# Kernel optimization log

Measured on AMD Instinct MI355X. Metric: run time of the kernel, lower is better.

The kernel has to match this reference:

```python
import jax, jax.numpy as jnp
import numpy as np

MARGIN = 1.0
N_NODES = 8192
EMBED_DIM = 128
N_COMM = 100


def setup_inputs() -> dict:
    key = jax.random.key(0)
    k1, k2 = jax.random.split(key)
    embeddings = jax.random.normal(k1, (N_NODES, EMBED_DIM), dtype=jnp.float32)
    communities = jax.random.randint(k2, (N_NODES,), 0, N_COMM, dtype=jnp.int64)
    return {"embeddings": embeddings, "communities": communities}


def _cdist(x):
    # Euclidean pairwise distances, sqrt made grad-safe at 0.
    sq = jnp.sum(x * x, axis=1)
    d2 = sq[:, None] + sq[None, :] - 2.0 * (x @ x.T)
    d2 = jnp.maximum(d2, 0.0)
    return jnp.where(d2 > 0, jnp.sqrt(jnp.where(d2 > 0, d2, 1.0)), 0.0)


def reference(embeddings, communities):
    n = embeddings.shape[0]
    dist = _cdist(embeddings)                              # (n, n)
    same = communities[:, None] == communities[None, :]    # (n, n)
    pos_mask = same & ~jnp.eye(n, dtype=bool)              # positives: same comm, j != i
    neg_mask = ~same                                       # negatives: any other community
    inf = jnp.array(jnp.inf, dist.dtype)
    # hardest (closest) negative per anchor row
    min_neg = jnp.min(jnp.where(neg_mask, dist, inf), axis=1)   # (n,)
    has_neg = jnp.any(neg_mask, axis=1)                         # (n,)
    # triplet margin over every (anchor, positive) pair
    tl = jnp.maximum(dist - min_neg[:, None] + MARGIN, 0.0)     # (n, n)
    valid = pos_mask & has_neg[:, None]
    total = jnp.sum(jnp.where(valid, tl, 0.0))
    count = jnp.sum(valid)
    # reduction='mean' over valid triplets; 0.0 if no valid triplets / single community
    return jnp.where(count > 0, total / count.astype(total.dtype), jnp.zeros((), total.dtype))
```

## Files before the change

### kernel.cpp

```cpp
#include <hip/hip_runtime.h>

#define N_NODES 8192
#define DIM     128
#define N_COMM  100
#define MARGIN  1.0f

#define KQ       32
#define LDS_STR  40
#define LDS_STRP 72
#define RP_STR   68

typedef __attribute__((ext_vector_type(8)))  short bf16x8;
typedef __attribute__((ext_vector_type(16))) float f32x16;

__device__ inline unsigned short f32_to_bf16_rne(float f) {
    unsigned u = __float_as_uint(f);
    unsigned r = u + 0x7fffu + ((u >> 16) & 1u);
    return (unsigned short)(r >> 16);
}
__device__ inline float bf16_to_f32(unsigned short h) {
    return __uint_as_float(((unsigned)h) << 16);
}

__global__ __launch_bounds__(256)
void prep_kernel(const float* __restrict__ x,
                 const int* __restrict__ comm,
                 unsigned short* __restrict__ xhi,
                 unsigned short* __restrict__ xlo,
                 float* __restrict__ sq,
                 unsigned int* __restrict__ min_d2,
                 int* __restrict__ offs,
                 int* __restrict__ members) {
    __shared__ int scnt[N_COMM];
    __shared__ int scur[N_COMM];
    const int tid = threadIdx.x;

    if (blockIdx.x < 2048) {
        int row  = blockIdx.x * 4 + (tid >> 6);
        int lane = tid & 63;
        const float* p = x + (size_t)row * DIM;
        float v0 = p[lane], v1 = p[lane + 64];
        unsigned short h0 = f32_to_bf16_rne(v0), h1 = f32_to_bf16_rne(v1);
        unsigned short l0 = f32_to_bf16_rne(v0 - bf16_to_f32(h0));
        unsigned short l1 = f32_to_bf16_rne(v1 - bf16_to_f32(h1));
        size_t base = (size_t)row * DIM;
        xhi[base + lane] = h0;  xhi[base + 64 + lane] = h1;
        xlo[base + lane] = l0;  xlo[base + 64 + lane] = l1;
        float s = v0 * v0 + v1 * v1;
        #pragma unroll
        for (int off = 32; off > 0; off >>= 1) s += __shfl_down(s, off);
        if (lane == 0) {
            sq[row] = s;
            min_d2[row] = 0x7f800000u;
        }
        return;
    }

    if (tid < N_COMM) scnt[tid] = 0;
    __syncthreads();
    for (int i = tid; i < N_NODES; i += 256) atomicAdd(&scnt[comm[i]], 1);
    __syncthreads();
    if (tid == 0) {
        int acc = 0;
        for (int c = 0; c < N_COMM; ++c) { scur[c] = acc; offs[c] = acc; acc += scnt[c]; }
        offs[N_COMM] = acc;
    }
    __syncthreads();
    for (int i = tid; i < N_NODES; i += 256) {
        int p = atomicAdd(&scur[comm[i]], 1);
        members[p] = i;
    }
}

__global__ __launch_bounds__(256, 3)
void minneg_mfma_kernel(const unsigned short* __restrict__ xhi,
                        const unsigned short* __restrict__ xlo,
                        const int* __restrict__ comm,
                        const float* __restrict__ sq,
                        unsigned int* __restrict__ min_d2) {
    __shared__ __align__(16) unsigned short lds[4][128][LDS_STR];
    __shared__ unsigned int colmin[128];

    const int b = blockIdx.x;
    int bx = (int)((sqrtf(8.f * (float)b + 1.f) - 1.f) * 0.5f);
    while ((bx + 1) * (bx + 2) / 2 <= b) ++bx;
    while (bx * (bx + 1) / 2 > b) --bx;
    const int by = b - bx * (bx + 1) / 2;

    const int tid  = threadIdx.x;
    const int lane = tid & 63;
    const int w    = tid >> 6;
    const int wr   = w >> 1, wc = w & 1;
    const int lr   = lane & 31;
    const int lh   = lane >> 5;
    const int i0   = bx * 128;
    const int j0   = by * 128;

    if (tid < 128) colmin[tid] = 0x7f800000u;

    f32x16 acc[2][2];
    #pragma unroll
    for (int g = 0; g < 2; ++g)
        #pragma unroll
        for (int h = 0; h < 2; ++h)
            #pragma unroll
            for (int e = 0; e < 16; ++e) acc[g][h][e] = 0.f;

    #pragma unroll
    for (int kq = 0; kq < 4; ++kq) {
        __syncthreads();
        #pragma unroll
        for (int it = 0; it < 8; ++it) {
            int g    = tid + it * 256;
            int tile = g >> 9;
            int row  = (g >> 2) & 127;
            int seg  = g & 3;
            const unsigned short* src = (tile & 1) ? xlo : xhi;
            int rbase = (tile & 2) ? j0 : i0;
            uint4 v = *(const uint4*)&src[(size_t)(rbase + row) * DIM + kq * KQ + seg * 8];
            *(uint4*)&lds[tile][row][seg * 8] = v;
        }
        __syncthreads();

        #pragma unroll
        for (int ks = 0; ks < 2; ++ks) {
            const int kb = ks * 16 + lh * 8;
            bf16x8 ahi[2], alo[2], bhi[2], blo[2];
            #pragma unroll
            for (int g = 0; g < 2; ++g) {
                ahi[g] = *(const bf16x8*)&lds[0][wr * 64 + g * 32 + lr][kb];
                alo[g] = *(const bf16x8*)&lds[1][wr * 64 + g * 32 + lr][kb];
            }
            #pragma unroll
            for (int h = 0; h < 2; ++h) {
                bhi[h] = *(const bf16x8*)&lds[2][wc * 64 + h * 32 + lr][kb];
                blo[h] = *(const bf16x8*)&lds[3][wc * 64 + h * 32 + lr][kb];
            }
            #pragma unroll
            for (int g = 0; g < 2; ++g)
                #pragma unroll
                for (int h = 0; h < 2; ++h) {
                    acc[g][h] = __builtin_amdgcn_mfma_f32_32x32x16_bf16(
                        ahi[g], bhi[h], acc[g][h], 0, 0, 0);
                    acc[g][h] = __builtin_amdgcn_mfma_f32_32x32x16_bf16(
                        ahi[g], blo[h], acc[g][h], 0, 0, 0);
                    acc[g][h] = __builtin_amdgcn_mfma_f32_32x32x16_bf16(
                        alo[g], bhi[h], acc[g][h], 0, 0, 0);
                }
        }
    }

    int   civ[2][4][4];
    float sqv[2][4][4];
    #pragma unroll
    for (int g = 0; g < 2; ++g)
        #pragma unroll
        for (int q = 0; q < 4; ++q) {
            int rb = i0 + wr * 64 + g * 32 + 4 * lh + 8 * q;
            *(int4*)&civ[g][q][0]   = *(const int4*)&comm[rb];
            *(float4*)&sqv[g][q][0] = *(const float4*)&sq[rb];
        }

    const float FINF = __uint_as_float(0x7f800000u);
    float rmin[2][16];
    #pragma unroll
    for (int g = 0; g < 2; ++g)
        #pragma unroll
        for (int e = 0; e < 16; ++e) rmin[g][e] = FINF;

    #pragma unroll
    for (int h = 0; h < 2; ++h) {
        int colt = wc * 64 + h * 32 + lr;
        int j  = j0 + colt;
        int cj = comm[j];
        float sqj = sq[j];
        float cmin = FINF;
        #pragma unroll
        for (int g = 0; g < 2; ++g)
            #pragma unroll
            for (int q = 0; q < 4; ++q)
                #pragma unroll
                for (int t = 0; t < 4; ++t) {
                    float d2 = fmaxf(sqv[g][q][t] + sqj - 2.f * acc[g][h][q * 4 + t], 0.f);
                    if (civ[g][q][t] != cj) {
                        cmin = fminf(cmin, d2);
                        rmin[g][q * 4 + t] = fminf(rmin[g][q * 4 + t], d2);
                    }
                }
        cmin = fminf(cmin, __shfl_xor(cmin, 32));
        if (lh == 0) atomicMin(&colmin[colt], __float_as_uint(cmin));
    }

    __syncthreads();
    float (*rowpart)[RP_STR] = (float (*)[RP_STR])lds;
    #pragma unroll
    for (int g = 0; g < 2; ++g)
        #pragma unroll
        for (int q = 0; q < 4; ++q)
            #pragma unroll
            for (int t = 0; t < 4; ++t) {
                int rowl = wr * 64 + g * 32 + 4 * lh + 8 * q + t;
                rowpart[rowl][wc * 32 + lr] = rmin[g][q * 4 + t];
            }
    __syncthreads();
    if (tid < 128) {
        float m = FINF;
        #pragma unroll
        for (int k = 0; k < 16; ++k) {
            float4 v = *(const float4*)&rowpart[tid][k * 4];
            m = fminf(m, fminf(fminf(v.x, v.y), fminf(v.z, v.w)));
        }
        atomicMin(&min_d2[i0 + tid], __float_as_uint(m));
        atomicMin(&min_d2[j0 + tid], colmin[tid]);
    }
}

__global__ __launch_bounds__(256, 2)
void pos_mfma_kernel(const unsigned short* __restrict__ xhi,
                     const unsigned short* __restrict__ xlo,
                     const float* __restrict__ sq,
                     const unsigned int* __restrict__ min_d2,
                     const int* __restrict__ offs,
                     const int* __restrict__ members,
                     double* __restrict__ psum,
                     unsigned int* __restrict__ pcnt) {
    __shared__ __align__(16) unsigned short lds[4][128][LDS_STRP];
    __shared__ float sqA[128], sqB[128], mnA[128];
    __shared__ double sred[4];
    __shared__ unsigned int cred[4];

    const int tid  = threadIdx.x;
    const int lane = tid & 63;
    const int w    = tid >> 6;
    const int wr   = w >> 1, wc = w & 1;
    const int lr   = lane & 31;
    const int lh   = lane >> 5;

    const int c    = blockIdx.x;
    const int beg  = offs[c], end = offs[c + 1];
    const int size = end - beg;
    const int nt   = (size + 127) >> 7;

    float tsum = 0.f;
    unsigned int tcnt = 0u;

    for (int tr = 0; tr < nt; ++tr)
    for (int tc = 0; tc < nt; ++tc) {
        bool av[2], bv[2];
        #pragma unroll
        for (int g = 0; g < 2; ++g) av[g] = (tr * 128 + wr * 64 + g * 32) < size;
        #pragma unroll
        for (int h = 0; h < 2; ++h) bv[h] = (tc * 128 + wc * 64 + h * 32) < size;

        __syncthreads();
        if (tid < 128) {
            int ii = beg + tr * 128 + tid;
            if (ii < end) {
                int ia = members[ii];
                sqA[tid] = sq[ia];
                unsigned int mb = min_d2[ia];
                mnA[tid] = (mb == 0x7f800000u) ? -1.f
                         : sqrtf(fmaxf(__uint_as_float(mb), 0.f));
            } else { sqA[tid] = 0.f; mnA[tid] = -1.f; }
        } else {
            int t2 = tid - 128;
            int jj = beg + tc * 128 + t2;
            sqB[t2] = (jj < end) ? sq[members[jj]] : 0.f;
        }

        f32x16 acc[2][2];
        #pragma unroll
        for (int g = 0; g < 2; ++g)
            #pragma unroll
            for (int h = 0; h < 2; ++h)
                #pragma unroll
                for (int e = 0; e < 16; ++e) acc[g][h][e] = 0.f;

        for (int kh = 0; kh < 2; ++kh) {
            __syncthreads();
            #pragma unroll
            for (int it = 0; it < 16; ++it) {
                int g    = tid + it * 256;
                int tile = g >> 10;
                int row  = (g >> 3) & 127;
                int seg  = g & 7;
                int mi   = beg + ((tile & 2) ? tc : tr) * 128 + row;
                int node = (mi < end) ? members[mi] : 0;
                const unsigned short* src = (tile & 1) ? xlo : xhi;
                uint4 v = *(const uint4*)&src[(size_t)node * DIM + kh * 64 + seg * 8];
                *(uint4*)&lds[tile][row][seg * 8] = v;
            }
            __syncthreads();

            #pragma unroll
            for (int ks = 0; ks < 4; ++ks) {
                const int kb = ks * 16 + lh * 8;
                bf16x8 ahi[2], alo[2], bhi[2], blo[2];
                #pragma unroll
                for (int g = 0; g < 2; ++g) if (av[g]) {
                    ahi[g] = *(const bf16x8*)&lds[0][wr * 64 + g * 32 + lr][kb];
                    alo[g] = *(const bf16x8*)&lds[1][wr * 64 + g * 32 + lr][kb];
                }
                #pragma unroll
                for (int h = 0; h < 2; ++h) if (bv[h]) {
                    bhi[h] = *(const bf16x8*)&lds[2][wc * 64 + h * 32 + lr][kb];
                    blo[h] = *(const bf16x8*)&lds[3][wc * 64 + h * 32 + lr][kb];
                }
                #pragma unroll
                for (int g = 0; g < 2; ++g)
                    #pragma unroll
                    for (int h = 0; h < 2; ++h) if (av[g] && bv[h]) {
                        acc[g][h] = __builtin_amdgcn_mfma_f32_32x32x16_bf16(
                            ahi[g], bhi[h], acc[g][h], 0, 0, 0);
                        acc[g][h] = __builtin_amdgcn_mfma_f32_32x32x16_bf16(
                            ahi[g], blo[h], acc[g][h], 0, 0, 0);
                        acc[g][h] = __builtin_amdgcn_mfma_f32_32x32x16_bf16(
                            alo[g], bhi[h], acc[g][h], 0, 0, 0);
                    }
            }
        }

        #pragma unroll
        for (int h = 0; h < 2; ++h) {
            if (!bv[h]) continue;
            int coll = wc * 64 + h * 32 + lr;
            int jv   = tc * 128 + coll;
            float sqj = sqB[coll];
            #pragma unroll
            for (int g = 0; g < 2; ++g) {
                if (!av[g]) continue;
                #pragma unroll
                for (int q = 0; q < 4; ++q)
                    #pragma unroll
                    for (int t = 0; t < 4; ++t) {
                        int rowl = wr * 64 + g * 32 + 4 * lh + 8 * q + t;
                        int iv   = tr * 128 + rowl;
                        float mn = mnA[rowl];
                        if (iv < size && jv < size && iv != jv && mn >= 0.f) {
                            float d2 = sqA[rowl] + sqj - 2.f * acc[g][h][q * 4 + t];
                            float dist = sqrtf(fmaxf(d2, 0.f));
                            tsum += fmaxf(dist - mn + MARGIN, 0.f);
                            tcnt += 1u;
                        }
                    }
            }
        }
    }

    #pragma unroll
    for (int off = 32; off > 0; off >>= 1) {
        tsum += __shfl_down(tsum, off);
        tcnt += __shfl_down(tcnt, off);
    }
    if (lane == 0) { sred[w] = (double)tsum; cred[w] = tcnt; }
    __syncthreads();
    if (tid == 0) {
        psum[c] = sred[0] + sred[1] + sred[2] + sred[3];
        pcnt[c] = cred[0] + cred[1] + cred[2] + cred[3];
    }
}

__global__ __launch_bounds__(256)
void finalize_kernel(const double* __restrict__ psum,
                     const unsigned int* __restrict__ pcnt,
                     float* __restrict__ out) {
    __shared__ double       ds[256];
    __shared__ unsigned int cs[256];
    const int t = threadIdx.x;
    double s = 0.0; unsigned int c = 0u;
    for (int b = t; b < N_COMM; b += 256) { s += psum[b]; c += pcnt[b]; }
    ds[t] = s; cs[t] = c;
    __syncthreads();
    for (int off = 128; off > 0; off >>= 1) {
        if (t < off) { ds[t] += ds[t + off]; cs[t] += cs[t + off]; }
        __syncthreads();
    }
    if (t == 0) out[0] = (cs[0] > 0u) ? (float)(ds[0] / (double)cs[0]) : 0.f;
}

extern "C" void kernel_launch(void* const* d_in, const int* in_sizes, int n_in,
                              void* d_out, int out_size, void* d_ws, size_t ws_size,
                              hipStream_t stream) {
    const float* x    = (const float*)d_in[0];
    const int*   comm = (const int*)d_in[1];
    float*       out  = (float*)d_out;

    char* ws = (char*)d_ws;
    float*          sq      = (float*)(ws);
    unsigned int*   min_d2  = (unsigned int*)(ws + 32768);
    int*            offs    = (int*)(ws + 65536);
    int*            members = (int*)(ws + 66048);
    double*         psum    = (double*)(ws + 98816);
    unsigned int*   pcnt    = (unsigned int*)(ws + 99840);
    unsigned short* xhi     = (unsigned short*)(ws + 100352);
    unsigned short* xlo     = (unsigned short*)(ws + 2197504);

    prep_kernel<<<2049, 256, 0, stream>>>(x, comm, xhi, xlo, sq, min_d2,
                                          offs, members);

    const int ntri = (N_NODES / 128) * (N_NODES / 128 + 1) / 2;
    minneg_mfma_kernel<<<ntri, 256, 0, stream>>>(xhi, xlo, comm, sq, min_d2);

    pos_mfma_kernel<<<N_COMM, 256, 0, stream>>>(xhi, xlo, sq, min_d2, offs, members,
                                                psum, pcnt);

    finalize_kernel<<<1, 256, 0, stream>>>(psum, pcnt, out);
}
```

Baseline: 134.8 us.

## Stage GEMM tiles via global_load_lds into fragment-ordered LDS layout

New measurement: 147.3 us. 1.09x slower.

```diff
diff --git a/kernel.cpp b/kernel.cpp
--- a/kernel.cpp
+++ b/kernel.cpp
@@ -5,10 +5,7 @@
 #define N_COMM  100
 #define MARGIN  1.0f
 
-#define KQ       32
-#define LDS_STR  40
 #define LDS_STRP 72
-#define RP_STR   68
 
 typedef __attribute__((ext_vector_type(8)))  short bf16x8;
 typedef __attribute__((ext_vector_type(16))) float f32x16;
@@ -78,8 +75,11 @@
                         const int* __restrict__ comm,
                         const float* __restrict__ sq,
                         unsigned int* __restrict__ min_d2) {
-    __shared__ __align__(16) unsigned short lds[4][128][LDS_STR];
+    __shared__ __align__(16) char smem[33792];
     __shared__ unsigned int colmin[128];
+    unsigned short (*frag)[4][2][64][8] =
+        (unsigned short (*)[4][2][64][8])smem;
+    float (*rowpart)[66] = (float (*)[66])smem;
 
     const int b = blockIdx.x;
     int bx = (int)((sqrtf(8.f * (float)b + 1.f) - 1.f) * 0.5f);
@@ -98,6 +98,10 @@
 
     if (tid < 128) colmin[tid] = 0x7f800000u;
 
+    const unsigned short* src   = (w & 1) ? xlo : xhi;
+    const int             rbw   = ((w & 2) ? j0 : i0) + lr;
+    const unsigned short* gbase = src + (size_t)rbw * DIM + lh * 8;
+
     f32x16 acc[2][2];
     #pragma unroll
     for (int g = 0; g < 2; ++g)
@@ -106,47 +110,59 @@
             #pragma unroll
             for (int e = 0; e < 16; ++e) acc[g][h][e] = 0.f;
 
-    #pragma unroll
     for (int kq = 0; kq < 4; ++kq) {
         __syncthreads();
         #pragma unroll
-        for (int it = 0; it < 8; ++it) {
-            int g    = tid + it * 256;
-            int tile = g >> 9;
-            int row  = (g >> 2) & 127;
-            int seg  = g & 3;
-            const unsigned short* src = (tile & 1) ? xlo : xhi;
-            int rbase = (tile & 2) ? j0 : i0;
-            uint4 v = *(const uint4*)&src[(size_t)(rbase + row) * DIM + kq * KQ + seg * 8];
-            *(uint4*)&lds[tile][row][seg * 8] = v;
-        }
+        for (int rg = 0; rg < 4; ++rg)
+            #pragma unroll
+            for (int kc = 0; kc < 2; ++kc) {
+                const unsigned short* g = gbase + kq * 32 + rg * 32 * DIM + kc * 16;
+                __builtin_amdgcn_global_load_lds(
+                    (const __attribute__((address_space(1))) void*)g,
+                    (__attribute__((address_space(3))) void*)&frag[w][rg][kc][0][0],
+                    16, 0, 0);
+            }
         __syncthreads();
 
         #pragma unroll
-        for (int ks = 0; ks < 2; ++ks) {
-            const int kb = ks * 16 + lh * 8;
-            bf16x8 ahi[2], alo[2], bhi[2], blo[2];
-            #pragma unroll
-            for (int g = 0; g < 2; ++g) {
-                ahi[g] = *(const bf16x8*)&lds[0][wr * 64 + g * 32 + lr][kb];
-                alo[g] = *(const bf16x8*)&lds[1][wr * 64 + g * 32 + lr][kb];
-            }
-            #pragma unroll
-            for (int h = 0; h < 2; ++h) {
-                bhi[h] = *(const bf16x8*)&lds[2][wc * 64 + h * 32 + lr][kb];
-                blo[h] = *(const bf16x8*)&lds[3][wc * 64 + h * 32 + lr][kb];
-            }
+        for (int kc = 0; kc < 2; ++kc) {
+            bf16x8 ahi[2], bhi[2];
             #pragma unroll
             for (int g = 0; g < 2; ++g)
-                #pragma unroll
-                for (int h = 0; h < 2; ++h) {
+                ahi[g] = *(const bf16x8*)&frag[0][wr * 2 + g][kc][lane][0];
+            #pragma unroll
+            for (int h = 0; h < 2; ++h)
+                bhi[h] = *(const bf16x8*)&frag[2][wc * 2 + h][kc][lane][0];
+            #pragma unroll
+            for (int g = 0; g < 2; ++g)
+                #pragma unroll
+                for (int h = 0; h < 2; ++h)
                     acc[g][h] = __builtin_amdgcn_mfma_f32_32x32x16_bf16(
                         ahi[g], bhi[h], acc[g][h], 0, 0, 0);
-                    acc[g][h] = __builtin_amdgcn_mfma_f32_32x32x16_bf16(
-                        ahi[g], blo[h], acc[g][h], 0, 0, 0);
-                    acc[g][h] = __builtin_amdgcn_mfma_f32_32x32x16_bf16(
-                        alo[g], bhi[h], acc[g][h], 0, 0, 0);
-                }
+            {
+                bf16x8 alo[2];
+                #pragma unroll
+                for (int g = 0; g < 2; ++g)
+                    alo[g] = *(const bf16x8*)&frag[1][wr * 2 + g][kc][lane][0];
+                #pragma unroll
+                for (int g = 0; g < 2; ++g)
+                    #pragma unroll
+                    for (int h = 0; h < 2; ++h)
+                        acc[g][h] = __builtin_amdgcn_mfma_f32_32x32x16_bf16(
+                            alo[g], bhi[h], acc[g][h], 0, 0, 0);
+            }
+            {
+                bf16x8 blo[2];
+                #pragma unroll
+                for (int h = 0; h < 2; ++h)
+                    blo[h] = *(const bf16x8*)&frag[3][wc * 2 + h][kc][lane][0];
+                #pragma unroll
+                for (int g = 0; g < 2; ++g)
+                    #pragma unroll
+                    for (int h = 0; h < 2; ++h)
+                        acc[g][h] = __builtin_amdgcn_mfma_f32_32x32x16_bf16(
+                            ahi[g], blo[h], acc[g][h], 0, 0, 0);
+            }
         }
     }
 
@@ -192,7 +208,6 @@
     }
 
     __syncthreads();
-    float (*rowpart)[RP_STR] = (float (*)[RP_STR])lds;
     #pragma unroll
     for (int g = 0; g < 2; ++g)
         #pragma unroll
```

## Preload full-K A fragments to registers and async-load B into LDS once

Applied to the files above, without the earlier changes.

Measured after the change: 163.7 us. 21.5% more time.

```diff
diff --git a/kernel.cpp b/kernel.cpp
--- a/kernel.cpp
+++ b/kernel.cpp
@@ -5,10 +5,7 @@
 #define N_COMM  100
 #define MARGIN  1.0f
 
-#define KQ       32
-#define LDS_STR  40
 #define LDS_STRP 72
-#define RP_STR   68
 
 typedef __attribute__((ext_vector_type(8)))  short bf16x8;
 typedef __attribute__((ext_vector_type(16))) float f32x16;
@@ -31,8 +28,6 @@
                  unsigned int* __restrict__ min_d2,
                  int* __restrict__ offs,
                  int* __restrict__ members) {
-    __shared__ int scnt[N_COMM];
-    __shared__ int scur[N_COMM];
     const int tid = threadIdx.x;
 
     if (blockIdx.x < 2048) {
@@ -56,30 +51,43 @@
         return;
     }
 
-    if (tid < N_COMM) scnt[tid] = 0;
-    __syncthreads();
-    for (int i = tid; i < N_NODES; i += 256) atomicAdd(&scnt[comm[i]], 1);
+    __shared__ int hist[N_COMM];
+    __shared__ int cursor;
+    const int c = blockIdx.x - 2048;
+    if (tid < N_COMM) hist[tid] = 0;
+    __syncthreads();
+    for (int i = tid; i < N_NODES; i += 256) atomicAdd(&hist[comm[i]], 1);
     __syncthreads();
     if (tid == 0) {
-        int acc = 0;
-        for (int c = 0; c < N_COMM; ++c) { scur[c] = acc; offs[c] = acc; acc += scnt[c]; }
-        offs[N_COMM] = acc;
+        int acc = 0, base = 0;
+        for (int cc = 0; cc < N_COMM; ++cc) {
+            if (cc == c) base = acc;
+            acc += hist[cc];
+        }
+        offs[c] = base;
+        if (c == N_COMM - 1) offs[N_COMM] = acc;
+        cursor = base;
     }
     __syncthreads();
     for (int i = tid; i < N_NODES; i += 256) {
-        int p = atomicAdd(&scur[comm[i]], 1);
-        members[p] = i;
-    }
-}
-
-__global__ __launch_bounds__(256, 3)
+        if (comm[i] == c) {
+            int p = atomicAdd(&cursor, 1);
+            members[p] = i;
+        }
+    }
+}
+
+__global__ __launch_bounds__(256, 2)
 void minneg_mfma_kernel(const unsigned short* __restrict__ xhi,
                         const unsigned short* __restrict__ xlo,
                         const int* __restrict__ comm,
                         const float* __restrict__ sq,
                         unsigned int* __restrict__ min_d2) {
-    __shared__ __align__(16) unsigned short lds[4][128][LDS_STR];
+    __shared__ __align__(16) char smem[65536];
     __shared__ unsigned int colmin[128];
+    unsigned short (*bfrag)[4][8][64][8] =
+        (unsigned short (*)[4][8][64][8])smem;
+    float (*rowpart)[66] = (float (*)[66])smem;
 
     const int b = blockIdx.x;
     int bx = (int)((sqrtf(8.f * (float)b + 1.f) - 1.f) * 0.5f);
@@ -98,6 +106,31 @@
 
     if (tid < 128) colmin[tid] = 0x7f800000u;
 
+    #pragma unroll
+    for (int pp = 0; pp < 2; ++pp) {
+        const int p  = w * 2 + pp;
+        const int hl = p >> 2, rg = p & 3;
+        const unsigned short* src = hl ? xlo : xhi;
+        const unsigned short* g0  = src + (size_t)(j0 + rg * 32 + lr) * DIM + lh * 8;
+        #pragma unroll
+        for (int ks = 0; ks < 8; ++ks)
+            __builtin_amdgcn_global_load_lds(
+                (const __attribute__((address_space(1))) void*)(g0 + ks * 16),
+                (__attribute__((address_space(3))) void*)&bfrag[hl][rg][ks][0][0],
+                16, 0, 0);
+    }
+
+    bf16x8 ahi[2][8], alo[2][8];
+    #pragma unroll
+    for (int g = 0; g < 2; ++g) {
+        const size_t rbase = (size_t)(i0 + wr * 64 + g * 32 + lr) * DIM + lh * 8;
+        #pragma unroll
+        for (int ks = 0; ks < 8; ++ks) {
+            ahi[g][ks] = *(const bf16x8*)&xhi[rbase + ks * 16];
+            alo[g][ks] = *(const bf16x8*)&xlo[rbase + ks * 16];
+        }
+    }
+
     f32x16 acc[2][2];
     #pragma unroll
     for (int g = 0; g < 2; ++g)
@@ -106,48 +139,27 @@
             #pragma unroll
             for (int e = 0; e < 16; ++e) acc[g][h][e] = 0.f;
 
-    #pragma unroll
-    for (int kq = 0; kq < 4; ++kq) {
-        __syncthreads();
-        #pragma unroll
-        for (int it = 0; it < 8; ++it) {
-            int g    = tid + it * 256;
-            int tile = g >> 9;
-            int row  = (g >> 2) & 127;
-            int seg  = g & 3;
-            const unsigned short* src = (tile & 1) ? xlo : xhi;
-            int rbase = (tile & 2) ? j0 : i0;
-            uint4 v = *(const uint4*)&src[(size_t)(rbase + row) * DIM + kq * KQ + seg * 8];
-            *(uint4*)&lds[tile][row][seg * 8] = v;
-        }
-        __syncthreads();
-
-        #pragma unroll
-        for (int ks = 0; ks < 2; ++ks) {
-            const int kb = ks * 16 + lh * 8;
-            bf16x8 ahi[2], alo[2], bhi[2], blo[2];
-            #pragma unroll
-            for (int g = 0; g < 2; ++g) {
-                ahi[g] = *(const bf16x8*)&lds[0][wr * 64 + g * 32 + lr][kb];
-                alo[g] = *(const bf16x8*)&lds[1][wr * 64 + g * 32 + lr][kb];
+    __syncthreads();
+
+    #pragma unroll
+    for (int ks = 0; ks < 8; ++ks) {
+        bf16x8 bhi[2], blo[2];
+        #pragma unroll
+        for (int h = 0; h < 2; ++h) {
+            bhi[h] = *(const bf16x8*)&bfrag[0][wc * 2 + h][ks][lane][0];
+            blo[h] = *(const bf16x8*)&bfrag[1][wc * 2 + h][ks][lane][0];
+        }
+        #pragma unroll
+        for (int g = 0; g < 2; ++g)
+            #pragma unroll
+            for (int h = 0; h < 2; ++h) {
+                acc[g][h] = __builtin_amdgcn_mfma_f32_32x32x16_bf16(
+                    ahi[g][ks], bhi[h], acc[g][h], 0, 0, 0);
+                acc[g][h] = __builtin_amdgcn_mfma_f32_32x32x16_bf16(
+                    alo[g][ks], bhi[h], acc[g][h], 0, 0, 0);
+                acc[g][h] = __builtin_amdgcn_mfma_f32_32x32x16_bf16(
+                    ahi[g][ks], blo[h], acc[g][h], 0, 0, 0);
             }
-            #pragma unroll
-            for (int h = 0; h < 2; ++h) {
-                bhi[h] = *(const bf16x8*)&lds[2][wc * 64 + h * 32 + lr][kb];
-                blo[h] = *(const bf16x8*)&lds[3][wc * 64 + h * 32 + lr][kb];
-            }
-            #pragma unroll
-            for (int g = 0; g < 2; ++g)
-                #pragma unroll
-                for (int h = 0; h < 2; ++h) {
-                    acc[g][h] = __builtin_amdgcn_mfma_f32_32x32x16_bf16(
-                        ahi[g], bhi[h], acc[g][h], 0, 0, 0);
-                    acc[g][h] = __builtin_amdgcn_mfma_f32_32x32x16_bf16(
-                        ahi[g], blo[h], acc[g][h], 0, 0, 0);
-                    acc[g][h] = __builtin_amdgcn_mfma_f32_32x32x16_bf16(
-                        alo[g], bhi[h], acc[g][h], 0, 0, 0);
-                }
-        }
     }
 
     int   civ[2][4][4];
@@ -192,7 +204,6 @@
     }
 
     __syncthreads();
-    float (*rowpart)[RP_STR] = (float (*)[RP_STR])lds;
     #pragma unroll
     for (int g = 0; g < 2; ++g)
         #pragma unroll
@@ -389,14 +400,14 @@
     float*          sq      = (float*)(ws);
     unsigned int*   min_d2  = (unsigned int*)(ws + 32768);
     int*            offs    = (int*)(ws + 65536);
-    int*            members = (int*)(ws + 66048);
-    double*         psum    = (double*)(ws + 98816);
-    unsigned int*   pcnt    = (unsigned int*)(ws + 99840);
-    unsigned short* xhi     = (unsigned short*)(ws + 100352);
-    unsigned short* xlo     = (unsigned short*)(ws + 2197504);
-
-    prep_kernel<<<2049, 256, 0, stream>>>(x, comm, xhi, xlo, sq, min_d2,
-                                          offs, members);
+    int*            members = (int*)(ws + 66560);
+    double*         psum    = (double*)(ws + 99328);
+    unsigned int*   pcnt    = (unsigned int*)(ws + 100352);
+    unsigned short* xhi     = (unsigned short*)(ws + 100864);
+    unsigned short* xlo     = (unsigned short*)(ws + 2198016);
+
+    prep_kernel<<<2048 + N_COMM, 256, 0, stream>>>(x, comm, xhi, xlo, sq, min_d2,
+                                                   offs, members);
 
     const int ntri = (N_NODES / 128) * (N_NODES / 128 + 1) / 2;
     minneg_mfma_kernel<<<ntri, 256, 0, stream>>>(xhi, xlo, comm, sq, min_d2);
```
